# Performance work log

Hardware: AMD Instinct MI355X
Metric: run time of the kernel (lower is better)

## Reference

```python
import jax, jax.numpy as jnp
import numpy as np

B, S, D, H = 4, 2048, 1024, 16
DK = D // H
DFF = 4 * D
EPS = 1e-5


def layernorm(x, g, b):
    mu = jnp.mean(x, axis=-1, keepdims=True)
    var = jnp.var(x, axis=-1, keepdims=True)
    return (x - mu) * jax.lax.rsqrt(var + EPS) * g + b


def setup_inputs() -> dict:
    key = jax.random.key(0)
    ks = jax.random.split(key, 16)
    s_d = 1.0 / np.sqrt(D)
    s_f = 1.0 / np.sqrt(DFF)
    return {
        "x": jax.random.normal(ks[0], (B, S, D), jnp.float32),
        # attention projections (qkv_bias=False); weights stored [in, out]
        "wq": jax.random.normal(ks[1], (D, D), jnp.float32) * s_d,
        "wk": jax.random.normal(ks[2], (D, D), jnp.float32) * s_d,
        "wv": jax.random.normal(ks[3], (D, D), jnp.float32) * s_d,
        "wo": jax.random.normal(ks[4], (D, D), jnp.float32) * s_d,
        "bo": jax.random.normal(ks[5], (D,), jnp.float32) * s_d,
        # feedforward
        "w1": jax.random.normal(ks[6], (D, DFF), jnp.float32) * s_d,
        "b1": jax.random.normal(ks[7], (DFF,), jnp.float32) * s_d,
        "w2": jax.random.normal(ks[8], (DFF, D), jnp.float32) * s_f,
        "b2": jax.random.normal(ks[9], (D,), jnp.float32) * s_f,
        # layernorms
        "g1": jnp.ones((D,), jnp.float32),
        "be1": jnp.zeros((D,), jnp.float32),
        "g2": jnp.ones((D,), jnp.float32),
        "be2": jnp.zeros((D,), jnp.float32),
    }


def reference(x, wq, wk, wv, wo, bo, w1, b1, w2, b2, g1, be1, g2, be2):
    # dropout is identity at inference
    shortcut = x
    h = layernorm(x, g1, be1)
    # multi-head causal attention (naive, materializes [B,H,S,S])
    q = (h @ wq).reshape(B, S, H, DK).transpose(0, 2, 1, 3)
    k = (h @ wk).reshape(B, S, H, DK).transpose(0, 2, 1, 3)
    v = (h @ wv).reshape(B, S, H, DK).transpose(0, 2, 1, 3)
    scores = jnp.einsum("bhqd,bhkd->bhqk", q, k)
    causal = jnp.triu(jnp.ones((S, S), bool), k=1)
    scores = jnp.where(causal, -jnp.inf, scores)
    attn = jax.nn.softmax(scores / np.sqrt(DK), axis=-1)
    out = jnp.einsum("bhqk,bhkd->bhqd", attn, v)
    out = out.transpose(0, 2, 1, 3).reshape(B, S, D)
    x = out @ wo + bo + shortcut
    shortcut = x
    h = layernorm(x, g2, be2)
    h = jax.nn.gelu(h @ w1 + b1, approximate=False) @ w2 + b2
    return h + shortcut
```

## Files before the change

### kernel.cpp

```cpp
#include <hip/hip_runtime.h>


typedef unsigned short ushort;
typedef __attribute__((ext_vector_type(8))) short bf16x8;
typedef __attribute__((ext_vector_type(4))) float f32x4;
typedef __attribute__((ext_vector_type(4))) unsigned short ushort4v;

#define B_ 4
#define S_ 2048
#define D_ 1024
#define H_ 16
#define DK_ 64
#define DFF_ 4096

__device__ __forceinline__ float b2f(ushort u){
  union { unsigned int i; float f; } x; x.i = ((unsigned int)u) << 16; return x.f;
}
__device__ __forceinline__ ushort f2b(float f){
  union { float f; unsigned int i; } x; x.f = f;
  return (ushort)((x.i + 0x7fffu + ((x.i >> 16) & 1u)) >> 16);
}

__device__ __forceinline__ f32x4 mfma16(bf16x8 a, bf16x8 b, f32x4 c){
  return __builtin_amdgcn_mfma_f32_16x16x32_bf16(a, b, c, 0, 0, 0);
}

__device__ __forceinline__ void gload16(const ushort* g, ushort* l){
  __builtin_amdgcn_global_load_lds(
      (const __attribute__((address_space(1))) void*)g,
      (__attribute__((address_space(3))) void*)l, 16, 0, 0);
}

__global__ void transpose_f32_bf16(const float* __restrict__ in,
                                   ushort* __restrict__ out, int K, int N){
  __shared__ ushort t[32][33];
  int k0 = blockIdx.y * 32, n0 = blockIdx.x * 32;
  for (int i = threadIdx.y; i < 32; i += 8)
    t[i][threadIdx.x] = f2b(in[(size_t)(k0 + i) * N + n0 + threadIdx.x]);
  __syncthreads();
  for (int i = threadIdx.y; i < 32; i += 8)
    out[(size_t)(n0 + i) * K + k0 + threadIdx.x] = t[threadIdx.x][i];
}

__global__ __launch_bounds__(256) void ln_f32(
    const float* __restrict__ x, const float* __restrict__ g,
    const float* __restrict__ be, ushort* __restrict__ out){
  int row = blockIdx.x; int t = threadIdx.x;
  const float* xr = x + (size_t)row * D_;
  float4 v = *(const float4*)(xr + t * 4);
  float s = v.x + v.y + v.z + v.w;
  float q = v.x*v.x + v.y*v.y + v.z*v.z + v.w*v.w;
  for (int off = 32; off; off >>= 1){
    s += __shfl_down(s, off);
    q += __shfl_down(q, off);
  }
  __shared__ float ss[4], sq[4];
  int wave = t >> 6, lane = t & 63;
  if (lane == 0){ ss[wave] = s; sq[wave] = q; }
  __syncthreads();
  float ts = ss[0] + ss[1] + ss[2] + ss[3];
  float tq = sq[0] + sq[1] + sq[2] + sq[3];
  float mu  = ts * (1.0f / D_);
  float var = tq * (1.0f / D_) - mu * mu;
  float rstd = rsqrtf(var + 1e-5f);
  float4 gv = *(const float4*)(g  + t * 4);
  float4 bv = *(const float4*)(be + t * 4);
  ushort4v o;
  o[0] = f2b((v.x - mu) * rstd * gv.x + bv.x);
  o[1] = f2b((v.y - mu) * rstd * gv.y + bv.y);
  o[2] = f2b((v.z - mu) * rstd * gv.z + bv.z);
  o[3] = f2b((v.w - mu) * rstd * gv.w + bv.w);
  *(ushort4v*)(out + (size_t)row * D_ + t * 4) = o;
}

template<int MODE>
__global__ __launch_bounds__(256) void gemm_bf16(
    const ushort* __restrict__ A, const ushort* __restrict__ Bt,
    void* __restrict__ C0, void* __restrict__ C1, void* __restrict__ C2,
    const float* __restrict__ bias, const float* __restrict__ resf,
    int M, int N, int K)
{
  __shared__ ushort As[128 * 32];
  __shared__ ushort Bs[128 * 32];
  int m0 = blockIdx.y * 128, n0 = blockIdx.x * 128;
  int t = threadIdx.x;
  int wv = t >> 6, lane = t & 63;
  int wr = wv >> 1, wc = wv & 1;
  int lg = lane >> 4, lr = lane & 15;
  int lrow = lane >> 2, lcol = (lane & 3) << 3;

  f32x4 acc[4][4];
  for (int i = 0; i < 4; i++)
    for (int j = 0; j < 4; j++) acc[i][j] = (f32x4){0.f, 0.f, 0.f, 0.f};

  int nkt = K >> 5;
  for (int kt = 0; kt < nkt; ++kt){
    __syncthreads();
    {
      const ushort* Ag = A  + (size_t)(m0 + wv * 16 + lrow) * K + (kt << 5) + lcol;
      const ushort* Bg = Bt + (size_t)(n0 + wv * 16 + lrow) * K + (kt << 5) + lcol;
      gload16(Ag,                    As + wv * 512);
      gload16(Ag + (size_t)64 * K,   As + 2048 + wv * 512);
      gload16(Bg,                    Bs + wv * 512);
      gload16(Bg + (size_t)64 * K,   Bs + 2048 + wv * 512);
    }
    __syncthreads();
    bf16x8 af[4], bfr[4];
    for (int i = 0; i < 4; i++)
      af[i]  = *(const bf16x8*)(As + (wr * 64 + i * 16 + lr) * 32 + lg * 8);
    for (int j = 0; j < 4; j++)
      bfr[j] = *(const bf16x8*)(Bs + (wc * 64 + j * 16 + lr) * 32 + lg * 8);
    for (int i = 0; i < 4; i++)
      for (int j = 0; j < 4; j++)
        acc[i][j] = mfma16(af[i], bfr[j], acc[i][j]);
  }

  for (int i = 0; i < 4; i++){
    int mb = m0 + wr * 64 + i * 16 + lg * 4;
    for (int j = 0; j < 4; j++){
      int ng = n0 + wc * 64 + j * 16 + lr;
      for (int r = 0; r < 4; r++){
        int mg = mb + r;
        float vacc = acc[i][j][r];
        if constexpr (MODE == 0){
          int b = mg >> 11, si = mg & 2047;
          int which = ng >> 10;
          int hh = (ng >> 6) & 15, dk = ng & 63;
          if (which == 0)
            ((ushort*)C0)[((((size_t)b * H_ + hh) * S_ + si) << 6) + dk] = f2b(vacc);
          else if (which == 1)
            ((ushort*)C1)[((((size_t)b * H_ + hh) * S_ + si) << 6) + dk] = f2b(vacc);
          else
            ((ushort*)C2)[((((size_t)b * H_ + hh) * DK_ + dk) << 11) + si] = f2b(vacc);
        } else if constexpr (MODE == 1){
          size_t idx = (size_t)mg * N + ng;
          ((float*)C0)[idx] = vacc + bias[ng] + resf[idx];
        } else {
          size_t idx = (size_t)mg * N + ng;
          float xv = vacc + bias[ng];
          float gel = xv * 0.5f * (1.0f + erff(xv * 0.70710678118f));
          ((ushort*)C0)[idx] = f2b(gel);
        }
      }
    }
  }
}

__global__ __launch_bounds__(256) void attn_fwd(
    const ushort* __restrict__ qg, const ushort* __restrict__ kg,
    const ushort* __restrict__ vg, ushort* __restrict__ outp)
{
  int h = blockIdx.y, b = blockIdx.z;
  int wave = threadIdx.x >> 6, lane = threadIdx.x & 63;
  int lg = lane >> 4, lr = lane & 15;
  int qbase = blockIdx.x * 64 + wave * 16;
  const ushort* qp = qg + (((size_t)b * H_ + h) * S_) * DK_;
  const ushort* kp = kg + (((size_t)b * H_ + h) * S_) * DK_;
  const ushort* vp = vg + (((size_t)b * H_ + h) * DK_) * S_;
  __shared__ ushort plds[4][16][32];

  bf16x8 aq0 = *(const bf16x8*)(qp + (size_t)(qbase + lr) * DK_ + lg * 8);
  bf16x8 aq1 = *(const bf16x8*)(qp + (size_t)(qbase + lr) * DK_ + 32 + lg * 8);

  float m[4], l[4];
  f32x4 oacc[4];
  for (int r = 0; r < 4; r++){ m[r] = -3.0e38f; l[r] = 0.f; }
  for (int c = 0; c < 4; c++) oacc[c] = (f32x4){0.f, 0.f, 0.f, 0.f};

  int nkt = (qbase + 15) / 32 + 1;
  for (int kt = 0; kt < nkt; ++kt){
    int kb = kt * 32;
    f32x4 s[2];
    for (int kk = 0; kk < 2; kk++){
      bf16x8 bk0 = *(const bf16x8*)(kp + (size_t)(kb + kk * 16 + lr) * DK_ + lg * 8);
      bf16x8 bk1 = *(const bf16x8*)(kp + (size_t)(kb + kk * 16 + lr) * DK_ + 32 + lg * 8);
      f32x4 z = (f32x4){0.f, 0.f, 0.f, 0.f};
      s[kk] = mfma16(aq0, bk0, z);
      s[kk] = mfma16(aq1, bk1, s[kk]);
    }
    bool domask = (kb + 31) > qbase;
    for (int kk = 0; kk < 2; kk++)
      for (int r = 0; r < 4; r++){
        float sv = s[kk][r] * 0.125f;
        if (domask){
          int qgl = qbase + lg * 4 + r;
          int kgl = kb + kk * 16 + lr;
          if (kgl > qgl) sv = -1.0e30f;
        }
        s[kk][r] = sv;
      }
    float p0[4], p1[4], alpha[4];
    for (int r = 0; r < 4; r++){
      float rm = fmaxf(s[0][r], s[1][r]);
      for (int off = 1; off < 16; off <<= 1) rm = fmaxf(rm, __shfl_xor(rm, off));
      float mnew = fmaxf(m[r], rm);
      alpha[r] = expf(m[r] - mnew);
      p0[r] = expf(s[0][r] - mnew);
      p1[r] = expf(s[1][r] - mnew);
      float rs = p0[r] + p1[r];
      for (int off = 1; off < 16; off <<= 1) rs += __shfl_xor(rs, off);
      l[r] = l[r] * alpha[r] + rs;
      m[r] = mnew;
    }
    for (int c = 0; c < 4; c++)
      for (int r = 0; r < 4; r++) oacc[c][r] *= alpha[r];
    for (int r = 0; r < 4; r++){
      plds[wave][lg * 4 + r][lr]      = f2b(p0[r]);
      plds[wave][lg * 4 + r][16 + lr] = f2b(p1[r]);
    }
    bf16x8 pa = *(const bf16x8*)(&plds[wave][lr][lg * 8]);
    for (int c = 0; c < 4; c++){
      bf16x8 bv = *(const bf16x8*)(vp + (size_t)(c * 16 + lr) * S_ + kb + lg * 8);
      oacc[c] = mfma16(pa, bv, oacc[c]);
    }
  }
  for (int c = 0; c < 4; c++)
    for (int r = 0; r < 4; r++){
      size_t row = (size_t)b * S_ + qbase + lg * 4 + r;
      outp[row * D_ + h * DK_ + c * 16 + lr] = f2b(oacc[c][r] / l[r]);
    }
}

extern "C" void kernel_launch(void* const* d_in, const int* in_sizes, int n_in,
                              void* d_out, int out_size, void* d_ws, size_t ws_size,
                              hipStream_t stream)
{
  const float* x   = (const float*)d_in[0];
  const float* wq  = (const float*)d_in[1];
  const float* wk  = (const float*)d_in[2];
  const float* wv  = (const float*)d_in[3];
  const float* wo  = (const float*)d_in[4];
  const float* bo  = (const float*)d_in[5];
  const float* w1  = (const float*)d_in[6];
  const float* b1  = (const float*)d_in[7];
  const float* w2  = (const float*)d_in[8];
  const float* b2  = (const float*)d_in[9];
  const float* g1  = (const float*)d_in[10];
  const float* be1 = (const float*)d_in[11];
  const float* g2  = (const float*)d_in[12];
  const float* be2 = (const float*)d_in[13];

  char* ws = (char*)d_ws;
  const size_t MB = 1ull << 20;
  ushort* wqkvT = (ushort*)(ws + 0 * MB);
  ushort* woT  = (ushort*)(ws + 6 * MB);
  ushort* w1T  = (ushort*)(ws + 8 * MB);
  ushort* w2T  = (ushort*)(ws + 16 * MB);
  ushort* hbuf = (ushort*)(ws + 24 * MB);
  ushort* qbuf = (ushort*)(ws + 40 * MB);
  ushort* kbuf = (ushort*)(ws + 56 * MB);
  ushort* vbuf = (ushort*)(ws + 72 * MB);
  float*  x2f  = (float*)(ws + 88 * MB);

  dim3 tb(32, 8);
  transpose_f32_bf16<<<dim3(32, 32), tb, 0, stream>>>(wq, wqkvT, 1024, 1024);
  transpose_f32_bf16<<<dim3(32, 32), tb, 0, stream>>>(wk, wqkvT + (1024ull*1024), 1024, 1024);
  transpose_f32_bf16<<<dim3(32, 32), tb, 0, stream>>>(wv, wqkvT + (2048ull*1024), 1024, 1024);
  transpose_f32_bf16<<<dim3(32, 32), tb, 0, stream>>>(wo, woT, 1024, 1024);
  transpose_f32_bf16<<<dim3(128, 32), tb, 0, stream>>>(w1, w1T, 1024, 4096);
  transpose_f32_bf16<<<dim3(32, 128), tb, 0, stream>>>(w2, w2T, 4096, 1024);

  ln_f32<<<8192, 256, 0, stream>>>(x, g1, be1, hbuf);

  gemm_bf16<0><<<dim3(24, 64), 256, 0, stream>>>(hbuf, wqkvT, qbuf, kbuf, vbuf,
                                                 nullptr, nullptr, 8192, 3072, 1024);

  attn_fwd<<<dim3(32, 16, 4), 256, 0, stream>>>(qbuf, kbuf, vbuf, hbuf);

  gemm_bf16<1><<<dim3(8, 64), 256, 0, stream>>>(hbuf, woT, x2f, nullptr, nullptr,
                                                bo, x, 8192, 1024, 1024);

  ln_f32<<<8192, 256, 0, stream>>>(x2f, g2, be2, kbuf);

  for (int c = 0; c < 4; ++c){
    const ushort* h2c = kbuf + (size_t)c * 2048 * 1024;
    float* outc = (float*)d_out + (size_t)c * 2048 * 1024;
    const float* x2c = x2f + (size_t)c * 2048 * 1024;
    gemm_bf16<2><<<dim3(32, 16), 256, 0, stream>>>(h2c, w1T, vbuf, nullptr, nullptr,
                                                   b1, nullptr, 2048, 4096, 1024);
    gemm_bf16<1><<<dim3(8, 16), 256, 0, stream>>>(vbuf, w2T, outc, nullptr, nullptr,
                                                  b2, x2c, 2048, 1024, 4096);
  }
}
```

Baseline: 1.731 ms.

## Stage K/V tiles in double-buffered LDS for attention and unchunk FFN GEMMs

The attention kernel now handles 128 queries per block (32 per wave), loads K and V tiles of 64 keys into double-buffered, XOR-swizzled shared memory with async loads, and reuses each tile across the four waves and two row groups instead of every wave reading K/V from global memory. The FFN is also launched as a single pair of GEMMs over all 8192 rows, using a new workspace buffer instead of four sequential chunks, which cuts launch count and improves occupancy. The cost is more LDS, more registers per thread, and a barrier per KV tile. Causal work imbalance across blocks also grows because each block now spans a larger query range.

```diff
diff --git a/kernel.cpp b/kernel.cpp
--- a/kernel.cpp
+++ b/kernel.cpp
@@ -146,6 +146,7 @@
   }
 }
 
+#define KVB 64
 __global__ __launch_bounds__(256) void attn_fwd(
     const ushort* __restrict__ qg, const ushort* __restrict__ kg,
     const ushort* __restrict__ vg, ushort* __restrict__ outp)
@@ -153,72 +154,137 @@
   int h = blockIdx.y, b = blockIdx.z;
   int wave = threadIdx.x >> 6, lane = threadIdx.x & 63;
   int lg = lane >> 4, lr = lane & 15;
-  int qbase = blockIdx.x * 64 + wave * 16;
+  int q0 = blockIdx.x * 128;
+  int qbase = q0 + wave * 32;
   const ushort* qp = qg + (((size_t)b * H_ + h) * S_) * DK_;
   const ushort* kp = kg + (((size_t)b * H_ + h) * S_) * DK_;
   const ushort* vp = vg + (((size_t)b * H_ + h) * DK_) * S_;
-  __shared__ ushort plds[4][16][32];
-
-  bf16x8 aq0 = *(const bf16x8*)(qp + (size_t)(qbase + lr) * DK_ + lg * 8);
-  bf16x8 aq1 = *(const bf16x8*)(qp + (size_t)(qbase + lr) * DK_ + 32 + lg * 8);
-
-  float m[4], l[4];
-  f32x4 oacc[4];
-  for (int r = 0; r < 4; r++){ m[r] = -3.0e38f; l[r] = 0.f; }
-  for (int c = 0; c < 4; c++) oacc[c] = (f32x4){0.f, 0.f, 0.f, 0.f};
-
-  int nkt = (qbase + 15) / 32 + 1;
+
+  __shared__ ushort Ks[2][KVB][64];
+  __shared__ ushort Vs[2][KVB][64];
+  __shared__ ushort Ps[4][2][16][64];
+
+  bf16x8 aq[2][2];
+#pragma unroll
+  for (int rg = 0; rg < 2; rg++)
+#pragma unroll
+    for (int c = 0; c < 2; c++)
+      aq[rg][c] = *(const bf16x8*)(qp + (size_t)(qbase + rg * 16 + lr) * DK_ + c * 32 + lg * 8);
+
+  float m[2][4], l[2][4];
+  f32x4 oacc[2][4];
+#pragma unroll
+  for (int rg = 0; rg < 2; rg++)
+#pragma unroll
+    for (int r = 0; r < 4; r++){ m[rg][r] = -3.0e38f; l[rg][r] = 0.f; }
+#pragma unroll
+  for (int rg = 0; rg < 2; rg++)
+#pragma unroll
+    for (int c = 0; c < 4; c++) oacc[rg][c] = (f32x4){0.f, 0.f, 0.f, 0.f};
+
+  int r8   = lane >> 3;
+  int srcc = ((lane & 7) ^ r8) << 3;
+  int swz  = (lr & 7) << 3;
+
+#pragma unroll
+  for (int j = 0; j < 2; j++){
+    int rowb = wave * 16 + j * 8;
+    gload16(kp + (size_t)(rowb + r8) * 64 + srcc,        &Ks[0][rowb][0]);
+    gload16(vp + (size_t)(rowb + r8) * S_ + srcc,        &Vs[0][rowb][0]);
+  }
+
+  int nkt = q0 / KVB + 2;
+  int cur = 0;
   for (int kt = 0; kt < nkt; ++kt){
-    int kb = kt * 32;
-    f32x4 s[2];
-    for (int kk = 0; kk < 2; kk++){
-      bf16x8 bk0 = *(const bf16x8*)(kp + (size_t)(kb + kk * 16 + lr) * DK_ + lg * 8);
-      bf16x8 bk1 = *(const bf16x8*)(kp + (size_t)(kb + kk * 16 + lr) * DK_ + 32 + lg * 8);
-      f32x4 z = (f32x4){0.f, 0.f, 0.f, 0.f};
-      s[kk] = mfma16(aq0, bk0, z);
-      s[kk] = mfma16(aq1, bk1, s[kk]);
+    int kb = kt * KVB;
+    __syncthreads();
+    if (kt + 1 < nkt){
+      int kb2 = kb + KVB;
+#pragma unroll
+      for (int j = 0; j < 2; j++){
+        int rowb = wave * 16 + j * 8;
+        gload16(kp + (size_t)(kb2 + rowb + r8) * 64 + srcc, &Ks[cur ^ 1][rowb][0]);
+        gload16(vp + (size_t)(rowb + r8) * S_ + kb2 + srcc, &Vs[cur ^ 1][rowb][0]);
+      }
     }
-    bool domask = (kb + 31) > qbase;
-    for (int kk = 0; kk < 2; kk++)
+    bf16x8 bk[4][2], bv[4][2];
+#pragma unroll
+    for (int kk = 0; kk < 4; kk++)
+#pragma unroll
+      for (int c = 0; c < 2; c++)
+        bk[kk][c] = *(const bf16x8*)&Ks[cur][kk * 16 + lr][(c * 32 + lg * 8) ^ swz];
+#pragma unroll
+    for (int c = 0; c < 4; c++)
+#pragma unroll
+      for (int c2 = 0; c2 < 2; c2++)
+        bv[c][c2] = *(const bf16x8*)&Vs[cur][c * 16 + lr][(c2 * 32 + lg * 8) ^ swz];
+
+#pragma unroll
+    for (int rg = 0; rg < 2; rg++){
+      f32x4 s[4];
+#pragma unroll
+      for (int kk = 0; kk < 4; kk++){
+        f32x4 z = (f32x4){0.f, 0.f, 0.f, 0.f};
+        s[kk] = mfma16(aq[rg][0], bk[kk][0], z);
+        s[kk] = mfma16(aq[rg][1], bk[kk][1], s[kk]);
+      }
+      int qrow0 = qbase + rg * 16 + lg * 4;
+      bool domask = (kb + KVB - 1) > qrow0;
+#pragma unroll
+      for (int kk = 0; kk < 4; kk++)
+#pragma unroll
+        for (int r = 0; r < 4; r++){
+          float sv = s[kk][r] * 0.125f;
+          if (domask && (kb + kk * 16 + lr) > (qrow0 + r)) sv = -1.0e30f;
+          s[kk][r] = sv;
+        }
+      float p[4][4];
+#pragma unroll
       for (int r = 0; r < 4; r++){
-        float sv = s[kk][r] * 0.125f;
-        if (domask){
-          int qgl = qbase + lg * 4 + r;
-          int kgl = kb + kk * 16 + lr;
-          if (kgl > qgl) sv = -1.0e30f;
+        float rm = fmaxf(fmaxf(s[0][r], s[1][r]), fmaxf(s[2][r], s[3][r]));
+#pragma unroll
+        for (int off = 1; off < 16; off <<= 1) rm = fmaxf(rm, __shfl_xor(rm, off));
+        float mnew = fmaxf(m[rg][r], rm);
+        float alpha = expf(m[rg][r] - mnew);
+        float rs = 0.f;
+#pragma unroll
+        for (int kk = 0; kk < 4; kk++){
+          p[kk][r] = expf(s[kk][r] - mnew);
+          rs += p[kk][r];
         }
-        s[kk][r] = sv;
-      }
-    float p0[4], p1[4], alpha[4];
-    for (int r = 0; r < 4; r++){
-      float rm = fmaxf(s[0][r], s[1][r]);
-      for (int off = 1; off < 16; off <<= 1) rm = fmaxf(rm, __shfl_xor(rm, off));
-      float mnew = fmaxf(m[r], rm);
-      alpha[r] = expf(m[r] - mnew);
-      p0[r] = expf(s[0][r] - mnew);
-      p1[r] = expf(s[1][r] - mnew);
-      float rs = p0[r] + p1[r];
-      for (int off = 1; off < 16; off <<= 1) rs += __shfl_xor(rs, off);
-      l[r] = l[r] * alpha[r] + rs;
-      m[r] = mnew;
+#pragma unroll
+        for (int off = 1; off < 16; off <<= 1) rs += __shfl_xor(rs, off);
+        l[rg][r] = l[rg][r] * alpha + rs;
+        m[rg][r] = mnew;
+#pragma unroll
+        for (int c = 0; c < 4; c++) oacc[rg][c][r] *= alpha;
+      }
+#pragma unroll
+      for (int kk = 0; kk < 4; kk++)
+#pragma unroll
+        for (int r = 0; r < 4; r++){
+          int prow = lg * 4 + r;
+          Ps[wave][rg][prow][(kk * 16 + lr) ^ ((prow & 7) << 3)] = f2b(p[kk][r]);
+        }
+      bf16x8 pa0 = *(const bf16x8*)&Ps[wave][rg][lr][(lg * 8) ^ swz];
+      bf16x8 pa1 = *(const bf16x8*)&Ps[wave][rg][lr][(32 + lg * 8) ^ swz];
+#pragma unroll
+      for (int c = 0; c < 4; c++){
+        oacc[rg][c] = mfma16(pa0, bv[c][0], oacc[rg][c]);
+        oacc[rg][c] = mfma16(pa1, bv[c][1], oacc[rg][c]);
+      }
     }
+    cur ^= 1;
+  }
+#pragma unroll
+  for (int rg = 0; rg < 2; rg++)
+#pragma unroll
     for (int c = 0; c < 4; c++)
-      for (int r = 0; r < 4; r++) oacc[c][r] *= alpha[r];
-    for (int r = 0; r < 4; r++){
-      plds[wave][lg * 4 + r][lr]      = f2b(p0[r]);
-      plds[wave][lg * 4 + r][16 + lr] = f2b(p1[r]);
-    }
-    bf16x8 pa = *(const bf16x8*)(&plds[wave][lr][lg * 8]);
-    for (int c = 0; c < 4; c++){
-      bf16x8 bv = *(const bf16x8*)(vp + (size_t)(c * 16 + lr) * S_ + kb + lg * 8);
-      oacc[c] = mfma16(pa, bv, oacc[c]);
-    }
-  }
-  for (int c = 0; c < 4; c++)
-    for (int r = 0; r < 4; r++){
-      size_t row = (size_t)b * S_ + qbase + lg * 4 + r;
-      outp[row * D_ + h * DK_ + c * 16 + lr] = f2b(oacc[c][r] / l[r]);
-    }
+#pragma unroll
+      for (int r = 0; r < 4; r++){
+        size_t row = (size_t)b * S_ + qbase + rg * 16 + lg * 4 + r;
+        outp[row * D_ + h * DK_ + c * 16 + lr] = f2b(oacc[rg][c][r] / l[rg][r]);
+      }
 }
 
 extern "C" void kernel_launch(void* const* d_in, const int* in_sizes, int n_in,
@@ -251,6 +317,7 @@
   ushort* kbuf = (ushort*)(ws + 56 * MB);
   ushort* vbuf = (ushort*)(ws + 72 * MB);
   float*  x2f  = (float*)(ws + 88 * MB);
+  ushort* a1   = (ushort*)(ws + 120 * MB);
 
   dim3 tb(32, 8);
   transpose_f32_bf16<<<dim3(32, 32), tb, 0, stream>>>(wq, wqkvT, 1024, 1024);
@@ -265,20 +332,15 @@
   gemm_bf16<0><<<dim3(24, 64), 256, 0, stream>>>(hbuf, wqkvT, qbuf, kbuf, vbuf,
                                                  nullptr, nullptr, 8192, 3072, 1024);
 
-  attn_fwd<<<dim3(32, 16, 4), 256, 0, stream>>>(qbuf, kbuf, vbuf, hbuf);
+  attn_fwd<<<dim3(16, 16, 4), 256, 0, stream>>>(qbuf, kbuf, vbuf, hbuf);
 
   gemm_bf16<1><<<dim3(8, 64), 256, 0, stream>>>(hbuf, woT, x2f, nullptr, nullptr,
                                                 bo, x, 8192, 1024, 1024);
 
   ln_f32<<<8192, 256, 0, stream>>>(x2f, g2, be2, kbuf);
 
-  for (int c = 0; c < 4; ++c){
-    const ushort* h2c = kbuf + (size_t)c * 2048 * 1024;
-    float* outc = (float*)d_out + (size_t)c * 2048 * 1024;
-    const float* x2c = x2f + (size_t)c * 2048 * 1024;
-    gemm_bf16<2><<<dim3(32, 16), 256, 0, stream>>>(h2c, w1T, vbuf, nullptr, nullptr,
-                                                   b1, nullptr, 2048, 4096, 1024);
-    gemm_bf16<1><<<dim3(8, 16), 256, 0, stream>>>(vbuf, w2T, outc, nullptr, nullptr,
-                                                  b2, x2c, 2048, 1024, 4096);
-  }
-}
+  gemm_bf16<2><<<dim3(32, 64), 256, 0, stream>>>(kbuf, w1T, a1, nullptr, nullptr,
+                                                 b1, nullptr, 8192, 4096, 1024);
+  gemm_bf16<1><<<dim3(8, 64), 256, 0, stream>>>(a1, w2T, d_out, nullptr, nullptr,
+                                                b2, x2f, 8192, 1024, 4096);
+}
```

Measured after the change: 1.422 ms. 1.22x faster.
